# Performance work log

Measured on AMD Instinct MI355X. Metric: run time of the kernel, lower is better.

The kernel has to match this reference:

```python
import jax, jax.numpy as jnp
import numpy as np

IN_DIM, K, D, ITERS, EPS = 512, 8, 128, 3, 1e-8
LN_EPS = 1e-5

def _ln(x, g, b):
    m = jnp.mean(x, axis=-1, keepdims=True)
    v = jnp.var(x, axis=-1, keepdims=True)
    return (x - m) * jax.lax.rsqrt(v + LN_EPS) * g + b

def setup_inputs() -> dict:
    key = jax.random.key(0)
    ks = jax.random.split(key, 16)
    B, C, H, W = 64, IN_DIM, 32, 32
    s = lambda fan: 1.0 / np.sqrt(fan)
    inp = {
        'x': jax.random.normal(ks[0], (B, C, H, W), jnp.float32),
        'noise': jax.random.normal(ks[1], (B, K, D), jnp.float32),
        'slot_mu': jax.random.normal(ks[2], (1, K, D), jnp.float32) * 0.02,
        'slot_log_sigma': jnp.zeros((1, K, D), jnp.float32),
        'Wp': jax.random.uniform(ks[3], (IN_DIM, D), jnp.float32, -s(IN_DIM), s(IN_DIM)),
        'bp': jnp.zeros((D,), jnp.float32),
        'g_in': jnp.ones((D,), jnp.float32), 'b_in': jnp.zeros((D,), jnp.float32),
        'Wq': jax.random.uniform(ks[4], (D, D), jnp.float32, -s(D), s(D)),
        'bq': jnp.zeros((D,), jnp.float32),
        'Wk': jax.random.uniform(ks[5], (D, D), jnp.float32, -s(D), s(D)),
        'bk': jnp.zeros((D,), jnp.float32),
        'Wv': jax.random.uniform(ks[6], (D, D), jnp.float32, -s(D), s(D)),
        'bv': jnp.zeros((D,), jnp.float32),
        'W_ih': jax.random.uniform(ks[7], (3 * D, D), jnp.float32, -s(D), s(D)),
        'W_hh': jax.random.uniform(ks[8], (3 * D, D), jnp.float32, -s(D), s(D)),
        'b_ih': jax.random.uniform(ks[9], (3 * D,), jnp.float32, -s(D), s(D)),
        'b_hh': jax.random.uniform(ks[10], (3 * D,), jnp.float32, -s(D), s(D)),
        'W1': jax.random.uniform(ks[11], (D, 2 * D), jnp.float32, -s(D), s(D)),
        'b1': jnp.zeros((2 * D,), jnp.float32),
        'W2': jax.random.uniform(ks[12], (2 * D, D), jnp.float32, -s(2 * D), s(2 * D)),
        'b2': jnp.zeros((D,), jnp.float32),
        'g_slots': jnp.ones((D,), jnp.float32), 'b_slots': jnp.zeros((D,), jnp.float32),
        'g_mlp': jnp.ones((D,), jnp.float32), 'b_mlp': jnp.zeros((D,), jnp.float32),
    }
    return inp

def reference(x, noise, slot_mu, slot_log_sigma, Wp, bp, g_in, b_in,
              Wq, bq, Wk, bk, Wv, bv, W_ih, W_hh, b_ih, b_hh,
              W1, b1, W2, b2, g_slots, b_slots, g_mlp, b_mlp):
    B, C, H, W = x.shape
    N = H * W
    scale = D ** -0.5
    x_flat = x.reshape(B, C, N).transpose(0, 2, 1)          # [B,N,C]
    inputs = _ln(x_flat @ Wp + bp, g_in, b_in)              # [B,N,D]
    slots = slot_mu + jnp.exp(slot_log_sigma) * noise       # [B,K,D]
    k = inputs @ Wk + bk                                    # k/v are loop-invariant
    v = inputs @ Wv + bv
    attn = None
    for _ in range(ITERS):
        slots_prev = slots
        q = _ln(slots, g_slots, b_slots) @ Wq + bq          # [B,K,D]
        logits = jnp.einsum('bkd,bnd->bkn', q, k) * scale
        attn = jax.nn.softmax(logits, axis=1)               # softmax over slots
        attn_norm = attn / (jnp.sum(attn, axis=-1, keepdims=True) + EPS)
        updates = jnp.einsum('bkn,bnd->bkd', attn_norm, v)  # [B,K,D]
        # GRUCell (PyTorch gate order r,z,n)
        u2 = updates.reshape(B * K, D)
        h = slots_prev.reshape(B * K, D)
        gx = u2 @ W_ih.T + b_ih
        gh = h @ W_hh.T + b_hh
        xr, xz, xn = jnp.split(gx, 3, axis=-1)
        hr, hz, hn = jnp.split(gh, 3, axis=-1)
        r = jax.nn.sigmoid(xr + hr)
        z = jax.nn.sigmoid(xz + hz)
        n = jnp.tanh(xn + r * hn)
        slots = ((1.0 - z) * n + z * h).reshape(B, K, D)
        hmid = jax.nn.gelu(_ln(slots, g_mlp, b_mlp) @ W1 + b1, approximate=False)
        slots = slots + hmid @ W2 + b2
    return slots, attn
```

## Files before the change

### kernel.cpp

```cpp
#include <hip/hip_runtime.h>
#include <hip/hip_bf16.h>
#include <math.h>

#define B_ 64
#define C_ 512
#define N_ 1024
#define D_ 128
#define K_ 8

typedef __attribute__((ext_vector_type(8))) short bf16x8;
typedef __attribute__((ext_vector_type(4))) float f32x4;
typedef unsigned short ushort_t;

__device__ __forceinline__ unsigned short f2bs(float f) {
    union { __hip_bfloat16 h; unsigned short s; } u;
    u.h = __float2bfloat16(f);
    return u.s;
}
__device__ __forceinline__ float bs2f(unsigned short s) {
    union { unsigned int u; float f; } v;
    v.u = ((unsigned int)s) << 16;
    return v.f;
}
__device__ __forceinline__ float sigmoidf_(float x) { return 1.0f / (1.0f + expf(-x)); }
__device__ __forceinline__ float gelu_exact(float x) {
    return 0.5f * x * (1.0f + erff(x * 0.7071067811865476f));
}

__global__ __launch_bounds__(256) void prep_weights(
    const float* __restrict__ Wp, const float* __restrict__ Wk,
    const float* __restrict__ Wv, const float* __restrict__ W_ih,
    const float* __restrict__ W_hh,
    ushort_t* __restrict__ WpT, ushort_t* __restrict__ WkT,
    ushort_t* __restrict__ WvT, float* __restrict__ WTih,
    float* __restrict__ WThh)
{
    int tid = blockIdx.x * 256 + threadIdx.x;
    {
        int c = tid >> 7, d = tid & 127;
        WpT[d * 512 + c] = f2bs(Wp[tid]);
    }
    if (tid < 16384) {
        int c = tid >> 7, d = tid & 127;
        WkT[d * 128 + c] = f2bs(Wk[tid]);
        WvT[d * 128 + c] = f2bs(Wv[tid]);
    }
    if (tid < 49152) {
        int j = tid >> 7, c = tid & 127;
        WTih[c * 384 + j] = W_ih[tid];
        WThh[c * 384 + j] = W_hh[tid];
    }
}

__global__ __launch_bounds__(256) void proj_ln_mfma(
    const float* __restrict__ x, const ushort_t* __restrict__ WpT,
    const float* __restrict__ bp, const float* __restrict__ g_in,
    const float* __restrict__ b_in, ushort_t* __restrict__ outb)
{
    __shared__ ushort_t Al[64 * 40];
    __shared__ ushort_t Bl[128 * 40];
    __shared__ float red[64][2][2];
    const int t = threadIdx.x;
    const int b = blockIdx.x >> 4;
    const int n0 = (blockIdx.x & 15) << 6;
    const int w = t >> 6, lane = t & 63;
    const int quad = lane >> 4, m = lane & 15;
    const int rowoff = (w >> 1) << 5;
    const int coloff = (w & 1) << 6;

    f32x4 acc[2][4];
#pragma unroll
    for (int r = 0; r < 2; ++r)
#pragma unroll
        for (int c = 0; c < 4; ++c) acc[r][c] = (f32x4){0.f, 0.f, 0.f, 0.f};

    const float* xb = x + (size_t)b * (C_ * N_);
    for (int c0 = 0; c0 < C_; c0 += 32) {
#pragma unroll
        for (int i = 0; i < 8; ++i) {
            int idx = t + (i << 8);
            int cc = idx >> 6, nn = idx & 63;
            Al[nn * 40 + cc] = f2bs(xb[(size_t)(c0 + cc) * N_ + n0 + nn]);
        }
#pragma unroll
        for (int i = 0; i < 2; ++i) {
            int idx = t + (i << 8);
            int d = idx >> 2, seg = idx & 3;
            *(bf16x8*)&Bl[d * 40 + seg * 8] =
                *(const bf16x8*)&WpT[d * 512 + c0 + seg * 8];
        }
        __syncthreads();
        bf16x8 af[2], bfr[4];
#pragma unroll
        for (int r = 0; r < 2; ++r)
            af[r] = *(const bf16x8*)&Al[(rowoff + 16 * r + m) * 40 + quad * 8];
#pragma unroll
        for (int c = 0; c < 4; ++c)
            bfr[c] = *(const bf16x8*)&Bl[(coloff + 16 * c + m) * 40 + quad * 8];
#pragma unroll
        for (int r = 0; r < 2; ++r)
#pragma unroll
            for (int c = 0; c < 4; ++c)
                acc[r][c] = __builtin_amdgcn_mfma_f32_16x16x32_bf16(af[r], bfr[c], acc[r][c], 0, 0, 0);
        __syncthreads();
    }
    float gv[4], bv[4], bpv[4];
#pragma unroll
    for (int c = 0; c < 4; ++c) {
        int col = coloff + 16 * c + m;
        bpv[c] = bp[col]; gv[c] = g_in[col]; bv[c] = b_in[col];
    }
#pragma unroll
    for (int r = 0; r < 2; ++r)
#pragma unroll
        for (int c = 0; c < 4; ++c)
#pragma unroll
            for (int g = 0; g < 4; ++g) acc[r][c][g] += bpv[c];

#pragma unroll
    for (int r = 0; r < 2; ++r) {
#pragma unroll
        for (int g = 0; g < 4; ++g) {
            float s = 0.f, s2 = 0.f;
#pragma unroll
            for (int c = 0; c < 4; ++c) { float v = acc[r][c][g]; s += v; s2 += v * v; }
#pragma unroll
            for (int off = 1; off < 16; off <<= 1) {
                s += __shfl_xor(s, off, 64);
                s2 += __shfl_xor(s2, off, 64);
            }
            if (m == 0) {
                int row = rowoff + 16 * r + quad * 4 + g;
                red[row][w & 1][0] = s;
                red[row][w & 1][1] = s2;
            }
        }
    }
    __syncthreads();
#pragma unroll
    for (int r = 0; r < 2; ++r) {
#pragma unroll
        for (int g = 0; g < 4; ++g) {
            int row = rowoff + 16 * r + quad * 4 + g;
            float s = red[row][0][0] + red[row][1][0];
            float s2 = red[row][0][1] + red[row][1][1];
            float mean = s * (1.f / 128.f);
            float var = s2 * (1.f / 128.f) - mean * mean;
            float rs = rsqrtf(var + 1e-5f);
            size_t base = ((size_t)b * N_ + n0 + row) * D_;
#pragma unroll
            for (int c = 0; c < 4; ++c) {
                int col = coloff + 16 * c + m;
                float v = (acc[r][c][g] - mean) * rs * gv[c] + bv[c];
                outb[base + col] = f2bs(v);
            }
        }
    }
}

__global__ __launch_bounds__(256) void kv_mfma(
    const ushort_t* __restrict__ A,
    const ushort_t* __restrict__ WkT, const float* __restrict__ bk,
    const ushort_t* __restrict__ WvT, const float* __restrict__ bv,
    ushort_t* __restrict__ kout, ushort_t* __restrict__ vout)
{
    __shared__ ushort_t Al[64 * 40];
    __shared__ ushort_t Bk[128 * 40];
    __shared__ ushort_t Bv[128 * 40];
    const int t = threadIdx.x;
    const int row0 = blockIdx.x << 6;
    const int w = t >> 6, lane = t & 63;
    const int quad = lane >> 4, m = lane & 15;
    const int is_v = w >> 1;
    const int rowoff = (w & 1) << 5;

    f32x4 acc[2][8];
#pragma unroll
    for (int r = 0; r < 2; ++r)
#pragma unroll
        for (int c = 0; c < 8; ++c) acc[r][c] = (f32x4){0.f, 0.f, 0.f, 0.f};

    for (int c0 = 0; c0 < D_; c0 += 32) {
#pragma unroll
        for (int i = 0; i < 2; ++i) {
            int idx = t + (i << 8);
            int rr = idx >> 3, cc4 = (idx & 7) << 2;
            *(ushort4*)&Al[rr * 40 + cc4] =
                *(const ushort4*)&A[(size_t)(row0 + rr) * D_ + c0 + cc4];
        }
#pragma unroll
        for (int i = 0; i < 2; ++i) {
            int idx = t + (i << 8);
            int d = idx >> 2, seg = idx & 3;
            *(bf16x8*)&Bk[d * 40 + seg * 8] =
                *(const bf16x8*)&WkT[d * 128 + c0 + seg * 8];
            *(bf16x8*)&Bv[d * 40 + seg * 8] =
                *(const bf16x8*)&WvT[d * 128 + c0 + seg * 8];
        }
        __syncthreads();
        const ushort_t* Bsrc = is_v ? Bv : Bk;
        bf16x8 af[2], bfr[8];
#pragma unroll
        for (int r = 0; r < 2; ++r)
            af[r] = *(const bf16x8*)&Al[(rowoff + 16 * r + m) * 40 + quad * 8];
#pragma unroll
        for (int c = 0; c < 8; ++c)
            bfr[c] = *(const bf16x8*)&Bsrc[(16 * c + m) * 40 + quad * 8];
#pragma unroll
        for (int r = 0; r < 2; ++r)
#pragma unroll
            for (int c = 0; c < 8; ++c)
                acc[r][c] = __builtin_amdgcn_mfma_f32_16x16x32_bf16(af[r], bfr[c], acc[r][c], 0, 0, 0);
        __syncthreads();
    }
    const float* bias = is_v ? bv : bk;
    ushort_t* dst = is_v ? vout : kout;
    float bval[8];
#pragma unroll
    for (int c = 0; c < 8; ++c) bval[c] = bias[16 * c + m];
#pragma unroll
    for (int r = 0; r < 2; ++r) {
#pragma unroll
        for (int g = 0; g < 4; ++g) {
            int row = rowoff + 16 * r + quad * 4 + g;
            size_t base = (size_t)(row0 + row) * D_;
#pragma unroll
            for (int c = 0; c < 8; ++c)
                dst[base + 16 * c + m] = f2bs(acc[r][c][g] + bval[c]);
        }
    }
}

__global__ __launch_bounds__(128) void init_q(
    const float* __restrict__ noise, const float* __restrict__ mu,
    const float* __restrict__ lsig,
    const float* __restrict__ g_slots, const float* __restrict__ b_slots,
    const float* __restrict__ Wq, const float* __restrict__ bq,
    float* __restrict__ slots, float* __restrict__ qbuf)
{
    __shared__ float sl[128], sl2[128];
    __shared__ float mrs[2];
    const int t = threadIdx.x;
    const int row = blockIdx.x;
    const int b = row >> 3;
    const int kd = (row & 7) * 128 + t;
    float sv = mu[kd] + expf(lsig[kd]) * noise[b * 1024 + kd];
    slots[(size_t)row * D_ + t] = sv;
    sl[t] = sv;
    __syncthreads();
    if (t < 64) {
        float v0 = sl[t], v1 = sl[t + 64];
        float s = v0 + v1, s2 = v0 * v0 + v1 * v1;
        for (int off = 32; off > 0; off >>= 1) {
            s += __shfl_down(s, off, 64);
            s2 += __shfl_down(s2, off, 64);
        }
        if (t == 0) {
            float mean = s * (1.f / 128.f);
            float var = s2 * (1.f / 128.f) - mean * mean;
            mrs[0] = mean; mrs[1] = rsqrtf(var + 1e-5f);
        }
    }
    __syncthreads();
    sl2[t] = (sl[t] - mrs[0]) * mrs[1] * g_slots[t] + b_slots[t];
    __syncthreads();
    float a = bq[t];
    for (int c = 0; c < 128; ++c) a = fmaf(sl2[c], Wq[(size_t)c * D_ + t], a);
    qbuf[(size_t)row * D_ + t] = a;
}

__global__ __launch_bounds__(512, 2) void attn_pv(
    const ushort_t* __restrict__ kb, const ushort_t* __restrict__ vb,
    const float* __restrict__ qbuf,
    float* __restrict__ S_part, float* __restrict__ upd_part,
    float* __restrict__ out_attn, int last)
{
    __shared__ __align__(16) char scratch[69632];
    __shared__ __align__(16) float at8[8][264];
    __shared__ __align__(16) float qs[8][132];
    __shared__ float red2[4][8];
    ushort_t* kvt = (ushort_t*)scratch;
    float* red = (float*)scratch;

    const int t = threadIdx.x;
    const int qd = blockIdx.x, b = blockIdx.y;
    const int nbase = qd << 8;
    const int wv = t >> 6, lane = t & 63;
    const float SCALE = 0.08838834764831845f;

    for (int i = t; i < 1024; i += 512)
        qs[i >> 7][i & 127] = qbuf[(size_t)b * 1024 + i];
#pragma unroll
    for (int i = 0; i < 8; ++i) {
        int idx = t + (i << 9);
        int rr = idx >> 4, u8 = (idx & 15) << 3;
        *(bf16x8*)&kvt[rr * 136 + u8] =
            *(const bf16x8*)&kb[((size_t)b * N_ + nbase + rr) * D_ + u8];
    }
    __syncthreads();

    {
        const int rr = t & 255, kh = t >> 8;
        float acc[4] = {0.f, 0.f, 0.f, 0.f};
        for (int c0 = 0; c0 < 128; c0 += 8) {
            bf16x8 kr = *(const bf16x8*)&kvt[rr * 136 + c0];
            float kf[8];
#pragma unroll
            for (int j = 0; j < 8; ++j) kf[j] = bs2f((ushort_t)kr[j]);
#pragma unroll
            for (int kk = 0; kk < 4; ++kk) {
                f32x4 qa = *(const f32x4*)&qs[4 * kh + kk][c0];
                f32x4 qb = *(const f32x4*)&qs[4 * kh + kk][c0 + 4];
                acc[kk] = fmaf(qa[0], kf[0], acc[kk]);
                acc[kk] = fmaf(qa[1], kf[1], acc[kk]);
                acc[kk] = fmaf(qa[2], kf[2], acc[kk]);
                acc[kk] = fmaf(qa[3], kf[3], acc[kk]);
                acc[kk] = fmaf(qb[0], kf[4], acc[kk]);
                acc[kk] = fmaf(qb[1], kf[5], acc[kk]);
                acc[kk] = fmaf(qb[2], kf[6], acc[kk]);
                acc[kk] = fmaf(qb[3], kf[7], acc[kk]);
            }
        }
#pragma unroll
        for (int kk = 0; kk < 4; ++kk)
            at8[4 * kh + kk][rr] = acc[kk];
    }
    __syncthreads();

    if (t < 256) {
        float l[8];
#pragma unroll
        for (int k = 0; k < 8; ++k) l[k] = at8[k][t] * SCALE;
        float mx = l[0];
#pragma unroll
        for (int k = 1; k < 8; ++k) mx = fmaxf(mx, l[k]);
        float e[8], ssum = 0.f;
#pragma unroll
        for (int k = 0; k < 8; ++k) { e[k] = expf(l[k] - mx); ssum += e[k]; }
        float inv = 1.f / ssum;
        float p[8];
#pragma unroll
        for (int k = 0; k < 8; ++k) {
            p[k] = e[k] * inv;
            at8[k][t] = p[k];
            if (last) out_attn[((size_t)b * K_ + k) * N_ + nbase + t] = p[k];
        }
#pragma unroll
        for (int k = 0; k < 8; ++k) {
            float v = p[k];
            for (int off = 32; off > 0; off >>= 1) v += __shfl_down(v, off, 64);
            if (lane == 0) red2[wv][k] = v;
        }
    }
    __syncthreads();
    if (t < 8)
        S_part[((size_t)b * 4 + qd) * 8 + t] =
            red2[0][t] + red2[1][t] + red2[2][t] + red2[3][t];

#pragma unroll
    for (int i = 0; i < 8; ++i) {
        int idx = t + (i << 9);
        int rr = idx >> 4, u8 = (idx & 15) << 3;
        *(bf16x8*)&kvt[rr * 136 + u8] =
            *(const bf16x8*)&vb[((size_t)b * N_ + nbase + rr) * D_ + u8];
    }
    __syncthreads();

    {
        float acc[8][4];
#pragma unroll
        for (int k = 0; k < 8; ++k)
#pragma unroll
            for (int j = 0; j < 4; ++j) acc[k][j] = 0.f;
        const int d4 = (t & 31) * 4, s = t >> 5;
#pragma unroll
        for (int i2 = 0; i2 < 4; ++i2) {
            const int nn = (s << 4) + (i2 << 2);
            float vf[4][4];
#pragma unroll
            for (int i = 0; i < 4; ++i) {
                ushort4 v4 = *(const ushort4*)&kvt[(nn + i) * 136 + d4];
                vf[i][0] = bs2f(v4.x); vf[i][1] = bs2f(v4.y);
                vf[i][2] = bs2f(v4.z); vf[i][3] = bs2f(v4.w);
            }
#pragma unroll
            for (int k = 0; k < 8; ++k) {
                f32x4 a4 = *(const f32x4*)&at8[k][nn];
#pragma unroll
                for (int i = 0; i < 4; ++i) {
                    acc[k][0] = fmaf(a4[i], vf[i][0], acc[k][0]);
                    acc[k][1] = fmaf(a4[i], vf[i][1], acc[k][1]);
                    acc[k][2] = fmaf(a4[i], vf[i][2], acc[k][2]);
                    acc[k][3] = fmaf(a4[i], vf[i][3], acc[k][3]);
                }
            }
        }
        __syncthreads();
#pragma unroll
        for (int k = 0; k < 8; ++k)
#pragma unroll
            for (int j = 0; j < 4; ++j)
                acc[k][j] += __shfl_xor(acc[k][j], 32, 64);
        if (lane < 32) {
#pragma unroll
            for (int k = 0; k < 8; ++k)
#pragma unroll
                for (int j = 0; j < 4; ++j)
                    red[(wv * 8 + k) * 132 + lane * 4 + j] = acc[k][j];
        }
        __syncthreads();
        for (int i = t; i < 1024; i += 512) {
            int k = i >> 7, d = i & 127;
            float ssum = 0.f;
#pragma unroll
            for (int w = 0; w < 8; ++w) ssum += red[(w * 8 + k) * 132 + d];
            upd_part[((size_t)b * 4 + qd) * 1024 + i] = ssum;
        }
    }
}

__global__ __launch_bounds__(256) void gru_mlp_q(
    const float* __restrict__ upd_part, const float* __restrict__ S_part,
    float* __restrict__ slots,
    const float* __restrict__ WTih, const float* __restrict__ WThh,
    const float* __restrict__ b_ih, const float* __restrict__ b_hh,
    const float* __restrict__ W1, const float* __restrict__ b1,
    const float* __restrict__ W2, const float* __restrict__ b2,
    const float* __restrict__ g_mlp, const float* __restrict__ b_mlp,
    const float* __restrict__ g_slots, const float* __restrict__ b_slots,
    const float* __restrict__ Wq, const float* __restrict__ bq,
    float* __restrict__ qbuf,
    float* __restrict__ out_slots, int final_iter)
{
    __shared__ float u[128], h[128], gx[384], gh[384], sn[128], tt[128], hm[256];
    __shared__ float mrs[2];
    const int t = threadIdx.x;
    const int row = blockIdx.x;
    const int b = row >> 3, k = row & 7;
    if (t < 128) {
        size_t sb = (size_t)b * 4;
        float S = S_part[(sb + 0) * 8 + k] + S_part[(sb + 1) * 8 + k]
                + S_part[(sb + 2) * 8 + k] + S_part[(sb + 3) * 8 + k];
        float inv = 1.0f / (S + 1e-8f);
        int i = k * 128 + t;
        float up = upd_part[(sb + 0) * 1024 + i] + upd_part[(sb + 1) * 1024 + i]
                 + upd_part[(sb + 2) * 1024 + i] + upd_part[(sb + 3) * 1024 + i];
        u[t] = up * inv;
        h[t] = slots[(size_t)row * D_ + t];
    }
    __syncthreads();
    {
        int j = t;
        float ax = 0.f, ah = 0.f;
        for (int c = 0; c < 128; ++c) {
            float uc = u[c], hc = h[c];
            ax = fmaf(uc, WTih[(size_t)c * 384 + j], ax);
            ah = fmaf(hc, WThh[(size_t)c * 384 + j], ah);
        }
        gx[j] = ax + b_ih[j];
        gh[j] = ah + b_hh[j];
    }
    if (t < 128) {
        int j = 256 + t;
        float ax = 0.f, ah = 0.f;
        for (int c = 0; c < 128; ++c) {
            float uc = u[c], hc = h[c];
            ax = fmaf(uc, WTih[(size_t)c * 384 + j], ax);
            ah = fmaf(hc, WThh[(size_t)c * 384 + j], ah);
        }
        gx[j] = ax + b_ih[j];
        gh[j] = ah + b_hh[j];
    }
    __syncthreads();
    if (t < 128) {
        float r = sigmoidf_(gx[t] + gh[t]);
        float z = sigmoidf_(gx[t + 128] + gh[t + 128]);
        float nv = tanhf(gx[t + 256] + r * gh[t + 256]);
        sn[t] = (1.0f - z) * nv + z * h[t];
    }
    __syncthreads();
    if (t < 64) {
        float v0 = sn[t], v1 = sn[t + 64];
        float s = v0 + v1, s2 = v0 * v0 + v1 * v1;
        for (int off = 32; off > 0; off >>= 1) {
            s += __shfl_down(s, off, 64);
            s2 += __shfl_down(s2, off, 64);
        }
        if (t == 0) {
            float mean = s * (1.f / 128.f);
            float var = s2 * (1.f / 128.f) - mean * mean;
            mrs[0] = mean; mrs[1] = rsqrtf(var + 1e-5f);
        }
    }
    __syncthreads();
    if (t < 128) tt[t] = (sn[t] - mrs[0]) * mrs[1] * g_mlp[t] + b_mlp[t];
    __syncthreads();
    {
        float a = 0.f;
        for (int c = 0; c < 128; ++c) a = fmaf(tt[c], W1[(size_t)c * 256 + t], a);
        hm[t] = gelu_exact(a + b1[t]);
    }
    __syncthreads();
    if (t < 128) {
        float a = sn[t] + b2[t];
        for (int j = 0; j < 256; ++j) a = fmaf(hm[j], W2[(size_t)j * D_ + t], a);
        slots[(size_t)row * D_ + t] = a;
        if (final_iter) out_slots[(size_t)row * D_ + t] = a;
        u[t] = a;
    }
    __syncthreads();
    if (t < 64) {
        float v0 = u[t], v1 = u[t + 64];
        float s = v0 + v1, s2 = v0 * v0 + v1 * v1;
        for (int off = 32; off > 0; off >>= 1) {
            s += __shfl_down(s, off, 64);
            s2 += __shfl_down(s2, off, 64);
        }
        if (t == 0) {
            float mean = s * (1.f / 128.f);
            float var = s2 * (1.f / 128.f) - mean * mean;
            mrs[0] = mean; mrs[1] = rsqrtf(var + 1e-5f);
        }
    }
    __syncthreads();
    if (t < 128) tt[t] = (u[t] - mrs[0]) * mrs[1] * g_slots[t] + b_slots[t];
    __syncthreads();
    if (!final_iter && t < 128) {
        float a = bq[t];
        for (int c = 0; c < 128; ++c) a = fmaf(tt[c], Wq[(size_t)c * D_ + t], a);
        qbuf[(size_t)row * D_ + t] = a;
    }
}

extern "C" void kernel_launch(void* const* d_in, const int* in_sizes, int n_in,
                              void* d_out, int out_size, void* d_ws, size_t ws_size,
                              hipStream_t stream) {
    const float* x       = (const float*)d_in[0];
    const float* noise   = (const float*)d_in[1];
    const float* slot_mu = (const float*)d_in[2];
    const float* slot_ls = (const float*)d_in[3];
    const float* Wp      = (const float*)d_in[4];
    const float* bp      = (const float*)d_in[5];
    const float* g_in    = (const float*)d_in[6];
    const float* b_in    = (const float*)d_in[7];
    const float* Wq      = (const float*)d_in[8];
    const float* bq      = (const float*)d_in[9];
    const float* Wk      = (const float*)d_in[10];
    const float* bk      = (const float*)d_in[11];
    const float* Wv      = (const float*)d_in[12];
    const float* bv      = (const float*)d_in[13];
    const float* W_ih    = (const float*)d_in[14];
    const float* W_hh    = (const float*)d_in[15];
    const float* b_ih    = (const float*)d_in[16];
    const float* b_hh    = (const float*)d_in[17];
    const float* W1      = (const float*)d_in[18];
    const float* b1      = (const float*)d_in[19];
    const float* W2      = (const float*)d_in[20];
    const float* b2      = (const float*)d_in[21];
    const float* g_slots = (const float*)d_in[22];
    const float* b_slots = (const float*)d_in[23];
    const float* g_mlp   = (const float*)d_in[24];
    const float* b_mlp   = (const float*)d_in[25];

    float* out_slots = (float*)d_out;
    float* out_attn  = (float*)d_out + 65536;

    float* wsf = (float*)d_ws;
    ushort_t* inputsb = (ushort_t*)wsf;
    ushort_t* kb = (ushort_t*)(wsf + 4194304);
    ushort_t* vb = (ushort_t*)(wsf + 8388608);
    float* slots    = wsf + 12582912;
    float* qbuf     = wsf + 12648448;
    float* upd_part = wsf + 12713984;
    float* S_part   = wsf + 12976128;
    ushort_t* WpT = (ushort_t*)(wsf + 13304320);
    ushort_t* WkT = (ushort_t*)(wsf + 13337088);
    ushort_t* WvT = (ushort_t*)(wsf + 13345280);
    float* WTih = wsf + 13353472;
    float* WThh = wsf + 13402624;

    prep_weights<<<dim3(256), dim3(256), 0, stream>>>(
        Wp, Wk, Wv, W_ih, W_hh, WpT, WkT, WvT, WTih, WThh);
    proj_ln_mfma<<<dim3(1024), dim3(256), 0, stream>>>(x, WpT, bp, g_in, b_in, inputsb);
    kv_mfma<<<dim3(1024), dim3(256), 0, stream>>>(inputsb, WkT, bk, WvT, bv, kb, vb);
    init_q<<<dim3(512), dim3(128), 0, stream>>>(
        noise, slot_mu, slot_ls, g_slots, b_slots, Wq, bq, slots, qbuf);

    for (int it = 0; it < 3; ++it) {
        int last = (it == 2) ? 1 : 0;
        attn_pv<<<dim3(4, 64), dim3(512), 0, stream>>>(
            kb, vb, qbuf, S_part, upd_part, out_attn, last);
        gru_mlp_q<<<dim3(512), dim3(256), 0, stream>>>(
            upd_part, S_part, slots, WTih, WThh, b_ih, b_hh,
            W1, b1, W2, b2, g_mlp, b_mlp, g_slots, b_slots,
            Wq, bq, qbuf, out_slots, last);
    }
}
```

Before: 407.9 us.

## Fuse input projection with K/V GEMM and merge weight prep with slot init

The LayerNorm'd projected inputs now stay in shared memory as a bf16 tile, and each block runs the K/V GEMMs on that tile directly. This removes the global write and re-read of the intermediate inputs buffer and one launch. Weight transposition and slot/q initialisation are merged into one kernel, and the x tile load switches to float4 vector reads. Shared memory per block grows, which may lower occupancy in the fused kernel.

```diff
diff --git a/kernel.cpp b/kernel.cpp
--- a/kernel.cpp
+++ b/kernel.cpp
@@ -27,38 +27,84 @@
     return 0.5f * x * (1.0f + erff(x * 0.7071067811865476f));
 }
 
-__global__ __launch_bounds__(256) void prep_weights(
+__global__ __launch_bounds__(256) void prep_init(
     const float* __restrict__ Wp, const float* __restrict__ Wk,
     const float* __restrict__ Wv, const float* __restrict__ W_ih,
     const float* __restrict__ W_hh,
+    const float* __restrict__ noise, const float* __restrict__ mu,
+    const float* __restrict__ lsig,
+    const float* __restrict__ g_slots, const float* __restrict__ b_slots,
+    const float* __restrict__ Wq, const float* __restrict__ bq,
     ushort_t* __restrict__ WpT, ushort_t* __restrict__ WkT,
     ushort_t* __restrict__ WvT, float* __restrict__ WTih,
-    float* __restrict__ WThh)
+    float* __restrict__ WThh,
+    float* __restrict__ slots, float* __restrict__ qbuf)
 {
-    int tid = blockIdx.x * 256 + threadIdx.x;
-    {
-        int c = tid >> 7, d = tid & 127;
-        WpT[d * 512 + c] = f2bs(Wp[tid]);
-    }
-    if (tid < 16384) {
-        int c = tid >> 7, d = tid & 127;
-        WkT[d * 128 + c] = f2bs(Wk[tid]);
-        WvT[d * 128 + c] = f2bs(Wv[tid]);
-    }
-    if (tid < 49152) {
-        int j = tid >> 7, c = tid & 127;
-        WTih[c * 384 + j] = W_ih[tid];
-        WThh[c * 384 + j] = W_hh[tid];
-    }
-}
-
-__global__ __launch_bounds__(256) void proj_ln_mfma(
+    __shared__ float sl2[2][128];
+    __shared__ float tt2[2][128];
+    __shared__ float mrs2[2][2];
+    const int t = threadIdx.x;
+
+    if (blockIdx.x < 256) {
+        int tid = blockIdx.x * 256 + t;
+        {
+            int c = tid >> 7, d = tid & 127;
+            WpT[d * 512 + c] = f2bs(Wp[tid]);
+        }
+        if (tid < 16384) {
+            int c = tid >> 7, d = tid & 127;
+            WkT[d * 128 + c] = f2bs(Wk[tid]);
+            WvT[d * 128 + c] = f2bs(Wv[tid]);
+        }
+        if (tid < 49152) {
+            int j = tid >> 7, c = tid & 127;
+            WTih[c * 384 + j] = W_ih[tid];
+            WThh[c * 384 + j] = W_hh[tid];
+        }
+        return;
+    }
+
+    const int lr = t >> 7, lt = t & 127;
+    const int row = ((blockIdx.x - 256) << 1) | lr;
+    const int b = row >> 3;
+    const int kd = (row & 7) * 128 + lt;
+    float sv = mu[kd] + expf(lsig[kd]) * noise[b * 1024 + kd];
+    slots[(size_t)row * D_ + lt] = sv;
+    sl2[lr][lt] = sv;
+    __syncthreads();
+    if (lt < 64) {
+        float v0 = sl2[lr][lt], v1 = sl2[lr][lt + 64];
+        float s = v0 + v1, s2 = v0 * v0 + v1 * v1;
+        for (int off = 32; off > 0; off >>= 1) {
+            s += __shfl_down(s, off, 64);
+            s2 += __shfl_down(s2, off, 64);
+        }
+        if (lt == 0) {
+            float mean = s * (1.f / 128.f);
+            float var = s2 * (1.f / 128.f) - mean * mean;
+            mrs2[lr][0] = mean; mrs2[lr][1] = rsqrtf(var + 1e-5f);
+        }
+    }
+    __syncthreads();
+    tt2[lr][lt] = (sl2[lr][lt] - mrs2[lr][0]) * mrs2[lr][1] * g_slots[lt] + b_slots[lt];
+    __syncthreads();
+    float a = bq[lt];
+    for (int c = 0; c < 128; ++c) a = fmaf(tt2[lr][c], Wq[(size_t)c * D_ + lt], a);
+    qbuf[(size_t)row * D_ + lt] = a;
+}
+
+__global__ __launch_bounds__(256) void proj_kv(
     const float* __restrict__ x, const ushort_t* __restrict__ WpT,
     const float* __restrict__ bp, const float* __restrict__ g_in,
-    const float* __restrict__ b_in, ushort_t* __restrict__ outb)
+    const float* __restrict__ b_in,
+    const ushort_t* __restrict__ WkT, const float* __restrict__ bk,
+    const ushort_t* __restrict__ WvT, const float* __restrict__ bv,
+    ushort_t* __restrict__ kout, ushort_t* __restrict__ vout)
 {
-    __shared__ ushort_t Al[64 * 40];
-    __shared__ ushort_t Bl[128 * 40];
+    __shared__ __align__(16) ushort_t Al[64 * 40];
+    __shared__ __align__(16) ushort_t Bl[128 * 40];
+    __shared__ __align__(16) ushort_t Bv2[128 * 40];
+    __shared__ __align__(16) ushort_t A2[64 * 136];
     __shared__ float red[64][2][2];
     const int t = threadIdx.x;
     const int b = blockIdx.x >> 4;
@@ -77,10 +123,15 @@
     const float* xb = x + (size_t)b * (C_ * N_);
     for (int c0 = 0; c0 < C_; c0 += 32) {
 #pragma unroll
-        for (int i = 0; i < 8; ++i) {
+        for (int i = 0; i < 2; ++i) {
             int idx = t + (i << 8);
-            int cc = idx >> 6, nn = idx & 63;
-            Al[nn * 40 + cc] = f2bs(xb[(size_t)(c0 + cc) * N_ + n0 + nn]);
+            int cc = idx >> 4;
+            int nn4 = (idx & 15) << 2;
+            float4 xv = *(const float4*)&xb[(size_t)(c0 + cc) * N_ + n0 + nn4];
+            Al[(nn4    ) * 40 + cc] = f2bs(xv.x);
+            Al[(nn4 + 1) * 40 + cc] = f2bs(xv.y);
+            Al[(nn4 + 2) * 40 + cc] = f2bs(xv.z);
+            Al[(nn4 + 3) * 40 + cc] = f2bs(xv.w);
         }
 #pragma unroll
         for (int i = 0; i < 2; ++i) {
@@ -104,11 +155,11 @@
                 acc[r][c] = __builtin_amdgcn_mfma_f32_16x16x32_bf16(af[r], bfr[c], acc[r][c], 0, 0, 0);
         __syncthreads();
     }
-    float gv[4], bv[4], bpv[4];
+    float gv[4], bvv[4], bpv[4];
 #pragma unroll
     for (int c = 0; c < 4; ++c) {
         int col = coloff + 16 * c + m;
-        bpv[c] = bp[col]; gv[c] = g_in[col]; bv[c] = b_in[col];
+        bpv[c] = bp[col]; gv[c] = g_in[col]; bvv[c] = b_in[col];
     }
 #pragma unroll
     for (int r = 0; r < 2; ++r)
@@ -147,62 +198,39 @@
             float mean = s * (1.f / 128.f);
             float var = s2 * (1.f / 128.f) - mean * mean;
             float rs = rsqrtf(var + 1e-5f);
-            size_t base = ((size_t)b * N_ + n0 + row) * D_;
 #pragma unroll
             for (int c = 0; c < 4; ++c) {
                 int col = coloff + 16 * c + m;
-                float v = (acc[r][c][g] - mean) * rs * gv[c] + bv[c];
-                outb[base + col] = f2bs(v);
+                float v = (acc[r][c][g] - mean) * rs * gv[c] + bvv[c];
+                A2[row * 136 + col] = f2bs(v);
             }
         }
     }
-}
-
-__global__ __launch_bounds__(256) void kv_mfma(
-    const ushort_t* __restrict__ A,
-    const ushort_t* __restrict__ WkT, const float* __restrict__ bk,
-    const ushort_t* __restrict__ WvT, const float* __restrict__ bv,
-    ushort_t* __restrict__ kout, ushort_t* __restrict__ vout)
-{
-    __shared__ ushort_t Al[64 * 40];
-    __shared__ ushort_t Bk[128 * 40];
-    __shared__ ushort_t Bv[128 * 40];
-    const int t = threadIdx.x;
-    const int row0 = blockIdx.x << 6;
-    const int w = t >> 6, lane = t & 63;
-    const int quad = lane >> 4, m = lane & 15;
+
     const int is_v = w >> 1;
-    const int rowoff = (w & 1) << 5;
-
-    f32x4 acc[2][8];
+    const int rowoff2 = (w & 1) << 5;
+    f32x4 acc2[2][8];
 #pragma unroll
     for (int r = 0; r < 2; ++r)
 #pragma unroll
-        for (int c = 0; c < 8; ++c) acc[r][c] = (f32x4){0.f, 0.f, 0.f, 0.f};
+        for (int c = 0; c < 8; ++c) acc2[r][c] = (f32x4){0.f, 0.f, 0.f, 0.f};
 
     for (int c0 = 0; c0 < D_; c0 += 32) {
-#pragma unroll
-        for (int i = 0; i < 2; ++i) {
-            int idx = t + (i << 8);
-            int rr = idx >> 3, cc4 = (idx & 7) << 2;
-            *(ushort4*)&Al[rr * 40 + cc4] =
-                *(const ushort4*)&A[(size_t)(row0 + rr) * D_ + c0 + cc4];
-        }
 #pragma unroll
         for (int i = 0; i < 2; ++i) {
             int idx = t + (i << 8);
             int d = idx >> 2, seg = idx & 3;
-            *(bf16x8*)&Bk[d * 40 + seg * 8] =
+            *(bf16x8*)&Bl[d * 40 + seg * 8] =
                 *(const bf16x8*)&WkT[d * 128 + c0 + seg * 8];
-            *(bf16x8*)&Bv[d * 40 + seg * 8] =
+            *(bf16x8*)&Bv2[d * 40 + seg * 8] =
                 *(const bf16x8*)&WvT[d * 128 + c0 + seg * 8];
         }
         __syncthreads();
-        const ushort_t* Bsrc = is_v ? Bv : Bk;
+        const ushort_t* Bsrc = is_v ? Bv2 : Bl;
         bf16x8 af[2], bfr[8];
 #pragma unroll
         for (int r = 0; r < 2; ++r)
-            af[r] = *(const bf16x8*)&Al[(rowoff + 16 * r + m) * 40 + quad * 8];
+            af[r] = *(const bf16x8*)&A2[(rowoff2 + 16 * r + m) * 136 + c0 + quad * 8];
 #pragma unroll
         for (int c = 0; c < 8; ++c)
             bfr[c] = *(const bf16x8*)&Bsrc[(16 * c + m) * 40 + quad * 8];
@@ -210,7 +238,7 @@
         for (int r = 0; r < 2; ++r)
 #pragma unroll
             for (int c = 0; c < 8; ++c)
-                acc[r][c] = __builtin_amdgcn_mfma_f32_16x16x32_bf16(af[r], bfr[c], acc[r][c], 0, 0, 0);
+                acc2[r][c] = __builtin_amdgcn_mfma_f32_16x16x32_bf16(af[r], bfr[c], acc2[r][c], 0, 0, 0);
         __syncthreads();
     }
     const float* bias = is_v ? bv : bk;
@@ -222,51 +250,13 @@
     for (int r = 0; r < 2; ++r) {
 #pragma unroll
         for (int g = 0; g < 4; ++g) {
-            int row = rowoff + 16 * r + quad * 4 + g;
-            size_t base = (size_t)(row0 + row) * D_;
+            int row = rowoff2 + 16 * r + quad * 4 + g;
+            size_t base = ((size_t)b * N_ + n0 + row) * D_;
 #pragma unroll
             for (int c = 0; c < 8; ++c)
-                dst[base + 16 * c + m] = f2bs(acc[r][c][g] + bval[c]);
-        }
-    }
-}
-
-__global__ __launch_bounds__(128) void init_q(
-    const float* __restrict__ noise, const float* __restrict__ mu,
-    const float* __restrict__ lsig,
-    const float* __restrict__ g_slots, const float* __restrict__ b_slots,
-    const float* __restrict__ Wq, const float* __restrict__ bq,
-    float* __restrict__ slots, float* __restrict__ qbuf)
-{
-    __shared__ float sl[128], sl2[128];
-    __shared__ float mrs[2];
-    const int t = threadIdx.x;
-    const int row = blockIdx.x;
-    const int b = row >> 3;
-    const int kd = (row & 7) * 128 + t;
-    float sv = mu[kd] + expf(lsig[kd]) * noise[b * 1024 + kd];
-    slots[(size_t)row * D_ + t] = sv;
-    sl[t] = sv;
-    __syncthreads();
-    if (t < 64) {
-        float v0 = sl[t], v1 = sl[t + 64];
-        float s = v0 + v1, s2 = v0 * v0 + v1 * v1;
-        for (int off = 32; off > 0; off >>= 1) {
-            s += __shfl_down(s, off, 64);
-            s2 += __shfl_down(s2, off, 64);
-        }
-        if (t == 0) {
-            float mean = s * (1.f / 128.f);
-            float var = s2 * (1.f / 128.f) - mean * mean;
-            mrs[0] = mean; mrs[1] = rsqrtf(var + 1e-5f);
-        }
-    }
-    __syncthreads();
-    sl2[t] = (sl[t] - mrs[0]) * mrs[1] * g_slots[t] + b_slots[t];
-    __syncthreads();
-    float a = bq[t];
-    for (int c = 0; c < 128; ++c) a = fmaf(sl2[c], Wq[(size_t)c * D_ + t], a);
-    qbuf[(size_t)row * D_ + t] = a;
+                dst[base + 16 * c + m] = f2bs(acc2[r][c][g] + bval[c]);
+        }
+    }
 }
 
 __global__ __launch_bounds__(512, 2) void attn_pv(
@@ -566,7 +556,6 @@
     float* out_attn  = (float*)d_out + 65536;
 
     float* wsf = (float*)d_ws;
-    ushort_t* inputsb = (ushort_t*)wsf;
     ushort_t* kb = (ushort_t*)(wsf + 4194304);
     ushort_t* vb = (ushort_t*)(wsf + 8388608);
     float* slots    = wsf + 12582912;
@@ -579,12 +568,12 @@
     float* WTih = wsf + 13353472;
     float* WThh = wsf + 13402624;
 
-    prep_weights<<<dim3(256), dim3(256), 0, stream>>>(
-        Wp, Wk, Wv, W_ih, W_hh, WpT, WkT, WvT, WTih, WThh);
-    proj_ln_mfma<<<dim3(1024), dim3(256), 0, stream>>>(x, WpT, bp, g_in, b_in, inputsb);
-    kv_mfma<<<dim3(1024), dim3(256), 0, stream>>>(inputsb, WkT, bk, WvT, bv, kb, vb);
-    init_q<<<dim3(512), dim3(128), 0, stream>>>(
-        noise, slot_mu, slot_ls, g_slots, b_slots, Wq, bq, slots, qbuf);
+    prep_init<<<dim3(512), dim3(256), 0, stream>>>(
+        Wp, Wk, Wv, W_ih, W_hh, noise, slot_mu, slot_ls,
+        g_slots, b_slots, Wq, bq,
+        WpT, WkT, WvT, WTih, WThh, slots, qbuf);
+    proj_kv<<<dim3(1024), dim3(256), 0, stream>>>(
+        x, WpT, bp, g_in, b_in, WkT, bk, WvT, bv, kb, vb);
 
     for (int it = 0; it < 3; ++it) {
         int last = (it == 2) ? 1 : 0;
```

New measurement: 396.1 us. 1.03x faster.
